# Performance work log

Measured on AMD Instinct MI355X. Metric: run time of the kernel, lower is better.

The kernel has to match this reference:

```python
import jax, jax.numpy as jnp
import numpy as np

NX, NY, C, B, P = 432, 496, 64, 4, 40000


def setup_inputs() -> dict:
    key = jax.random.key(0)
    k1, _ = jax.random.split(key)
    pillar_features = jax.random.normal(k1, (P, C), dtype=jnp.float32)
    # Build voxel_coords with unique (x, y) cells per batch element so the
    # scatter-write has no duplicate indices (matches deterministic torch assignment).
    rng = np.random.default_rng(0)
    per = P // B  # pillars per sample
    coords = np.empty((P, 3), dtype=np.int64)
    for b in range(B):
        flat = rng.choice(NX * NY, size=per, replace=False)
        coords[b * per:(b + 1) * per, 0] = flat % NX          # x index
        coords[b * per:(b + 1) * per, 1] = flat // NX         # y index
        coords[b * per:(b + 1) * per, 2] = b                  # batch index (last col)
    return {
        "pillar_features": pillar_features,
        "voxel_coords": jnp.asarray(coords),
        "batch_size": B,
        "nx": NX,
        "ny": NY,
    }


def reference(pillar_features, voxel_coords, batch_size, nx, ny):
    # Fused scatter: compute a global flat index (batch, y, x) for every pillar
    # and scatter all pillars in a single pass (no per-batch masking loop).
    x = voxel_coords[:, 0]
    y = voxel_coords[:, 1]
    b = voxel_coords[:, -1]
    flat = b * (ny * nx) + y * nx + x                       # [P]
    c = pillar_features.shape[1]
    grid = jnp.zeros((batch_size * ny * nx, c), dtype=pillar_features.dtype)
    grid = grid.at[flat].set(pillar_features)               # scatter pillars
    # [B*ny*nx, C] -> [B, C, ny, nx]
    return grid.reshape(batch_size, ny, nx, c).transpose(0, 3, 1, 2)
```

## Files before the change

kernel.cpp:

```cpp
#include <hip/hip_runtime.h>


#define C_CH 64

__global__ void build_map_kernel(const int* __restrict__ coords, int n_pillars,
                                 const int* __restrict__ nx_p,
                                 const int* __restrict__ ny_p,
                                 int* __restrict__ map) {
    int p = blockIdx.x * blockDim.x + threadIdx.x;
    if (p >= n_pillars) return;
    const int nx = nx_p[0];
    const int ny = ny_p[0];
    const int x = coords[3 * p + 0];
    const int y = coords[3 * p + 1];
    const int b = coords[3 * p + 2];
    const long long m = (long long)b * (long long)(nx * ny) + (long long)y * nx + x;
    map[m] = p;
}

__global__ void gather64_kernel(const float* __restrict__ feat,
                                const int* __restrict__ map,
                                const int* __restrict__ nx_p,
                                const int* __restrict__ ny_p,
                                float* __restrict__ out, int n_map) {
    const int tid = blockIdx.x * blockDim.x + threadIdx.x;
    if (tid >= n_map) return;
    const int plane = nx_p[0] * ny_p[0];
    const int b = tid / plane;
    const int rem = tid - b * plane;
    const size_t base = (size_t)b * C_CH * (size_t)plane + (size_t)rem;

    const int p = map[tid];

    float vals[C_CH];
#pragma unroll
    for (int c = 0; c < C_CH; ++c) vals[c] = 0.0f;

    if (p >= 0) {
        const float4* __restrict__ src =
            (const float4*)(feat + (size_t)p * C_CH);
#pragma unroll
        for (int i = 0; i < C_CH / 4; ++i) {
            float4 v = src[i];
            vals[4 * i + 0] = v.x;
            vals[4 * i + 1] = v.y;
            vals[4 * i + 2] = v.z;
            vals[4 * i + 3] = v.w;
        }
    }

#pragma unroll
    for (int c = 0; c < C_CH; ++c) {
        out[base + (size_t)c * (size_t)plane] = vals[c];
    }
}

__global__ void direct_scatter_kernel(const float* __restrict__ feat,
                                      const int* __restrict__ coords,
                                      int n_pillars, int C,
                                      const int* __restrict__ nx_p,
                                      const int* __restrict__ ny_p,
                                      float* __restrict__ out) {
    const long long t = (long long)blockIdx.x * blockDim.x + threadIdx.x;
    if (t >= (long long)n_pillars * C) return;
    const int p = (int)(t / C);
    const int c = (int)(t - (long long)p * C);
    const int nx = nx_p[0];
    const int ny = ny_p[0];
    const int x = coords[3 * p + 0];
    const int y = coords[3 * p + 1];
    const int b = coords[3 * p + 2];
    const int plane = nx * ny;
    const size_t o = ((size_t)b * C + c) * (size_t)plane + (size_t)y * nx + x;
    out[o] = feat[(size_t)p * C + c];
}

extern "C" void kernel_launch(void* const* d_in, const int* in_sizes, int n_in,
                              void* d_out, int out_size, void* d_ws, size_t ws_size,
                              hipStream_t stream) {
    const float* feat   = (const float*)d_in[0];
    const int*   coords = (const int*)d_in[1];
    const int* nx_p = (const int*)d_in[3];
    const int* ny_p = (const int*)d_in[4];
    float* out = (float*)d_out;

    const int n_pillars = in_sizes[1] / 3;
    const int C = in_sizes[0] / n_pillars;
    const int n_map = out_size / C;
    const size_t map_bytes = (size_t)n_map * sizeof(int);

    if (C == C_CH && ws_size >= map_bytes) {
        int* map = (int*)d_ws;
        hipMemsetAsync(map, 0xFF, map_bytes, stream);
        build_map_kernel<<<(n_pillars + 255) / 256, 256, 0, stream>>>(
            coords, n_pillars, nx_p, ny_p, map);
        gather64_kernel<<<(n_map + 255) / 256, 256, 0, stream>>>(
            feat, map, nx_p, ny_p, out, n_map);
    } else {
        hipMemsetAsync(out, 0, (size_t)out_size * sizeof(float), stream);
        const long long total = (long long)n_pillars * C;
        direct_scatter_kernel<<<(unsigned)((total + 255) / 256), 256, 0, stream>>>(
            feat, coords, n_pillars, C, nx_p, ny_p, out);
    }
}
```

Measured before the change: 232.9 us.

## Gather four cells per thread with float4 nontemporal stores to output

```diff
diff --git a/kernel.cpp b/kernel.cpp
--- a/kernel.cpp
+++ b/kernel.cpp
@@ -2,6 +2,8 @@
 
 
 #define C_CH 64
+
+typedef float nat_float4 __attribute__((ext_vector_type(4)));
 
 __global__ void build_map_kernel(const int* __restrict__ coords, int n_pillars,
                                  const int* __restrict__ nx_p,
@@ -18,40 +20,36 @@
     map[m] = p;
 }
 
-__global__ void gather64_kernel(const float* __restrict__ feat,
-                                const int* __restrict__ map,
-                                const int* __restrict__ nx_p,
-                                const int* __restrict__ ny_p,
-                                float* __restrict__ out, int n_map) {
-    const int tid = blockIdx.x * blockDim.x + threadIdx.x;
-    if (tid >= n_map) return;
-    const int plane = nx_p[0] * ny_p[0];
-    const int b = tid / plane;
-    const int rem = tid - b * plane;
-    const size_t base = (size_t)b * C_CH * (size_t)plane + (size_t)rem;
+__global__ void __launch_bounds__(256) gather64x4_kernel(
+        const float* __restrict__ feat,
+        const int* __restrict__ map,
+        const int* __restrict__ nx_p,
+        const int* __restrict__ ny_p,
+        float* __restrict__ out, int n_cell4) {
+    const int t = blockIdx.x * blockDim.x + threadIdx.x;
+    if (t >= n_cell4) return;
+    const int plane4 = (nx_p[0] * ny_p[0]) >> 2;
+    const int b = t / plane4;
+    const int rem4 = t - b * plane4;
 
-    const int p = map[tid];
+    const int4 pv = ((const int4*)map)[t];
 
-    float vals[C_CH];
-#pragma unroll
-    for (int c = 0; c < C_CH; ++c) vals[c] = 0.0f;
+    const float* __restrict__ f0 = feat + (long long)pv.x * C_CH;
+    const float* __restrict__ f1 = feat + (long long)pv.y * C_CH;
+    const float* __restrict__ f2 = feat + (long long)pv.z * C_CH;
+    const float* __restrict__ f3 = feat + (long long)pv.w * C_CH;
 
-    if (p >= 0) {
-        const float4* __restrict__ src =
-            (const float4*)(feat + (size_t)p * C_CH);
-#pragma unroll
-        for (int i = 0; i < C_CH / 4; ++i) {
-            float4 v = src[i];
-            vals[4 * i + 0] = v.x;
-            vals[4 * i + 1] = v.y;
-            vals[4 * i + 2] = v.z;
-            vals[4 * i + 3] = v.w;
-        }
-    }
+    nat_float4* __restrict__ out4 = (nat_float4*)out;
+    const int base = b * C_CH * plane4 + rem4;
 
-#pragma unroll
+#pragma unroll 8
     for (int c = 0; c < C_CH; ++c) {
-        out[base + (size_t)c * (size_t)plane] = vals[c];
+        nat_float4 v = {0.f, 0.f, 0.f, 0.f};
+        if (pv.x >= 0) v.x = f0[c];
+        if (pv.y >= 0) v.y = f1[c];
+        if (pv.z >= 0) v.z = f2[c];
+        if (pv.w >= 0) v.w = f3[c];
+        __builtin_nontemporal_store(v, out4 + base + c * plane4);
     }
 }
 
@@ -89,15 +87,16 @@
     const int n_map = out_size / C;
     const size_t map_bytes = (size_t)n_map * sizeof(int);
 
-    if (C == C_CH && ws_size >= map_bytes) {
+    if (C == C_CH && (n_map & 3) == 0 && ws_size >= map_bytes) {
         int* map = (int*)d_ws;
-        hipMemsetAsync(map, 0xFF, map_bytes, stream);
+        (void)hipMemsetAsync(map, 0xFF, map_bytes, stream);
         build_map_kernel<<<(n_pillars + 255) / 256, 256, 0, stream>>>(
             coords, n_pillars, nx_p, ny_p, map);
-        gather64_kernel<<<(n_map + 255) / 256, 256, 0, stream>>>(
-            feat, map, nx_p, ny_p, out, n_map);
+        const int n_cell4 = n_map >> 2;
+        gather64x4_kernel<<<(n_cell4 + 255) / 256, 256, 0, stream>>>(
+            feat, map, nx_p, ny_p, out, n_cell4);
     } else {
-        hipMemsetAsync(out, 0, (size_t)out_size * sizeof(float), stream);
+        (void)hipMemsetAsync(out, 0, (size_t)out_size * sizeof(float), stream);
         const long long total = (long long)n_pillars * C;
         direct_scatter_kernel<<<(unsigned)((total + 255) / 256), 256, 0, stream>>>(
             feat, coords, n_pillars, C, nx_p, ny_p, out);
```

Measured after the change: 242.1 us. 1.04x slower.
